# Kernel optimization log

Hardware: AMD Instinct MI355X
Metric: run time of the kernel (lower is better)

The kernel has to match this reference:

```python
import jax, jax.numpy as jnp
import numpy as np

N, IN_F, OUT_F, H = 4096, 256, 512, 8
D = OUT_F // H  # hidden per head
NEG_SLOPE = 0.2


def setup_inputs() -> dict:
    key = jax.random.key(0)
    k1, k2, k3 = jax.random.split(key, 3)
    inp = jax.random.normal(k1, (N, IN_F), dtype=jnp.float32)
    A = jnp.zeros((N, N), dtype=jnp.float32)  # additive adjacency mask
    # xavier_uniform for W [out, in]
    limW = float(np.sqrt(6.0 / (IN_F + H * D)))
    W = jax.random.uniform(k2, (H * D, IN_F), minval=-limW, maxval=limW, dtype=jnp.float32)
    lima = float(np.sqrt(6.0 / (H * D + 1)))
    a_left = jax.random.uniform(k3, (1, H, D), minval=-lima, maxval=lima, dtype=jnp.float32)
    return {"inp": inp, "A": A, "W": W, "a_left": a_left}


def reference(inp, A, W, a_left):
    # h: [N, H, D]
    h = (inp @ W.T).reshape(-1, H, D)
    # NOTE: source uses a_left for BOTH source and target scores (a_right is dead code)
    scores = jnp.sum(h * a_left, axis=-1)  # [N, H]
    s = scores.T  # [H, N]
    # [H, N, N] additive attention logits
    logits = jax.nn.leaky_relu(s[:, :, None] + s[:, None, :], negative_slope=NEG_SLOPE)
    logits = logits + A[None, :, :]
    att = jax.nn.softmax(logits, axis=-1)  # [H, N, N]
    # bmm: [H,N,N] x [H,N,D] -> [H,N,D] -> [N,H,D]
    out = jnp.einsum('hij,jhd->ihd', att, h)
    return out.reshape(-1, H * D)
```

## Files before the change

kernel.cpp:

```cpp
#include <hip/hip_runtime.h>
#include <math.h>

#define N 4096
#define IN_F 256
#define OUT_F 512
#define H 8
#define D 64
#define NEG 0.2f
#define JC 2048

typedef __attribute__((ext_vector_type(8))) short bf16x8;
typedef __attribute__((ext_vector_type(4))) float f32x4;

__device__ __forceinline__ float leaky(float x) { return fmaxf(x, NEG * x); }

__device__ __forceinline__ unsigned short f2bf(float x) {
    union { float f; unsigned u; } v; v.f = x;
    unsigned r = v.u + 0x7fff + ((v.u >> 16) & 1);
    return (unsigned short)(r >> 16);
}

__device__ __forceinline__ unsigned fmap(float x) {
    union { float f; unsigned u; } v; v.f = x;
    return (v.u & 0x80000000u) ? ~v.u : (v.u | 0x80000000u);
}
__device__ __forceinline__ float funmap(unsigned m) {
    union { float f; unsigned u; } v;
    v.u = (m & 0x80000000u) ? (m & 0x7fffffffu) : ~m;
    return v.f;
}

__device__ __forceinline__ void dma16(const void* g, void* l) {
    __builtin_amdgcn_global_load_lds((const __attribute__((address_space(1))) void*)g,
                                     (__attribute__((address_space(3))) void*)l, 16, 0, 0);
}

__global__ __launch_bounds__(256) void k_gemm(const float* __restrict__ inp,
                                              const float* __restrict__ W,
                                              const float* __restrict__ a_left,
                                              unsigned short* __restrict__ hbT,
                                              float* __restrict__ s,
                                              unsigned* __restrict__ smaxU) {
    __shared__ float As[64][68];
    __shared__ float Bs[64][68];
    __shared__ unsigned short h_st[64][72];
    __shared__ float s_red[64];

    const int t = threadIdx.x;
    const int bi = blockIdx.x;
    const int head = blockIdx.y;
    const int ty = t >> 4, tx = t & 15;
    const int lr = t >> 2;
    const int cq = (t & 3) * 16;

    float4 pa[4], pb[4];
    auto loadrk = [&](int k0) {
        const float* ip = &inp[(size_t)(bi * 64 + lr) * IN_F + k0 + cq];
        const float* wp = &W[(size_t)(head * 64 + lr) * IN_F + k0 + cq];
#pragma unroll
        for (int q = 0; q < 4; ++q) {
            pa[q] = *(const float4*)&ip[q * 4];
            pb[q] = *(const float4*)&wp[q * 4];
        }
    };
    loadrk(0);

    float acc[4][4] = {};
    for (int k0 = 0; k0 < IN_F; k0 += 64) {
        __syncthreads();
#pragma unroll
        for (int q = 0; q < 4; ++q)
#pragma unroll
            for (int j = 0; j < 4; ++j) {
                As[cq + q * 4 + j][lr] = ((const float*)&pa[q])[j];
                Bs[cq + q * 4 + j][lr] = ((const float*)&pb[q])[j];
            }
        __syncthreads();
        if (k0 + 64 < IN_F) loadrk(k0 + 64);
#pragma unroll
        for (int k = 0; k < 64; ++k) {
            float4 a4 = *(const float4*)&As[k][ty * 4];
            float4 b4 = *(const float4*)&Bs[k][tx * 4];
            float a[4] = {a4.x, a4.y, a4.z, a4.w};
            float b[4] = {b4.x, b4.y, b4.z, b4.w};
#pragma unroll
            for (int r = 0; r < 4; ++r)
#pragma unroll
                for (int c = 0; c < 4; ++c) acc[r][c] = fmaf(a[r], b[c], acc[r][c]);
        }
    }

    float aL[4];
#pragma unroll
    for (int c = 0; c < 4; ++c) aL[c] = a_left[head * D + tx * 4 + c];
#pragma unroll
    for (int r = 0; r < 4; ++r) {
        float sp = acc[r][0] * aL[0] + acc[r][1] * aL[1] + acc[r][2] * aL[2] + acc[r][3] * aL[3];
        sp += __shfl_xor(sp, 1); sp += __shfl_xor(sp, 2);
        sp += __shfl_xor(sp, 4); sp += __shfl_xor(sp, 8);
        if (tx == 0) {
            s[head * N + bi * 64 + ty * 4 + r] = sp;
            s_red[ty * 4 + r] = sp;
        }
    }
    __syncthreads();
    if (t < 64) {
        float m = s_red[t];
        for (int off = 32; off; off >>= 1) m = fmaxf(m, __shfl_down(m, off, 64));
        if (t == 0) atomicMax(&smaxU[head], fmap(m));
    }

#pragma unroll
    for (int r = 0; r < 4; ++r) {
        ushort4 v;
        v.x = f2bf(acc[r][0]); v.y = f2bf(acc[r][1]);
        v.z = f2bf(acc[r][2]); v.w = f2bf(acc[r][3]);
        *(ushort4*)&h_st[ty * 4 + r][tx * 4] = v;
    }
    __syncthreads();
    {
        const int d = t >> 2, iq = (t & 3) * 16;
        unsigned short us[16];
#pragma unroll
        for (int k = 0; k < 16; ++k) us[k] = h_st[iq + k][d];
        unsigned short* dst = &hbT[((size_t)(head * D + d)) * N + bi * 64 + iq];
#pragma unroll
        for (int q = 0; q < 4; ++q) {
            ushort4 v = {us[q * 4 + 0], us[q * 4 + 1], us[q * 4 + 2], us[q * 4 + 3]};
            *(ushort4*)&dst[q * 4] = v;
        }
    }
}

__global__ __launch_bounds__(256) void k_rowmax(const float* __restrict__ A,
                                                float* __restrict__ rmax) {
    int i = blockIdx.x;
    const float* row = &A[(size_t)i * N];
    float m = -1e30f;
    for (int j = threadIdx.x * 4; j < N; j += 256 * 4) {
        float4 v = *(const float4*)&row[j];
        m = fmaxf(fmaxf(fmaxf(m, v.x), fmaxf(v.y, v.z)), v.w);
    }
    for (int off = 32; off; off >>= 1) m = fmaxf(m, __shfl_down(m, off, 64));
    __shared__ float red[4];
    if ((threadIdx.x & 63) == 0) red[threadIdx.x >> 6] = m;
    __syncthreads();
    if (threadIdx.x == 0) rmax[i] = fmaxf(fmaxf(red[0], red[1]), fmaxf(red[2], red[3]));
}

__global__ __launch_bounds__(256, 4) void k_attn(const float* __restrict__ A,
                                                 const unsigned short* __restrict__ hbT,
                                                 const float* __restrict__ s,
                                                 const unsigned* __restrict__ smaxU,
                                                 const float* __restrict__ rmax,
                                                 float* __restrict__ out,
                                                 float* __restrict__ Z) {
    __shared__ float A_st[64 * 16 * 4];
    __shared__ unsigned short hT_st[64 * 8 * 8];
    __shared__ float s_ch[JC];

    const int t = threadIdx.x;
    const int i0 = blockIdx.x * 64;
    const int head = blockIdx.y;
    const int j0 = blockIdx.z * JC;
    const int lane = t & 63, wave = t >> 6, quad = lane >> 4, li = lane & 15;
    const int iw = wave * 16;
    const int myrow = i0 + iw + li;

#pragma unroll
    for (int q = 0; q < 2; ++q) {
        int idx = q * 256 + t;
        *(float4*)&s_ch[idx * 4] = *(const float4*)&s[head * N + j0 + idx * 4];
    }
    const float s_i = s[head * N + myrow];
    const float mb = leaky(s_i + funmap(smaxU[head])) + rmax[myrow];

    const float* gA[4]; void* lA[4];
#pragma unroll
    for (int q = 0; q < 4; ++q) {
        int slot = q * 256 + t;
        int r = slot >> 4, c4p = slot & 15;
        int c4 = c4p ^ (r & 7);
        gA[q] = &A[(size_t)(i0 + r) * N + j0 + c4 * 4];
        lA[q] = (void*)&A_st[slot * 4];
    }
    const unsigned short* gH[2]; void* lH[2];
#pragma unroll
    for (int q = 0; q < 2; ++q) {
        int slot = q * 256 + t;
        int r = slot >> 3, u = slot & 7;
        int uc = u ^ (r & 7);
        gH[q] = &hbT[(size_t)head * D * N + (size_t)r * N + j0 + uc * 8];
        lH[q] = (void*)&hT_st[slot * 8];
    }

    f32x4 acc[4] = {{0, 0, 0, 0}, {0, 0, 0, 0}, {0, 0, 0, 0}, {0, 0, 0, 0}};
    float zsum = 0.f;

    for (int jt = 0; jt < JC; jt += 64) {
        __syncthreads();
#pragma unroll
        for (int q = 0; q < 4; ++q) dma16(gA[q] + jt, lA[q]);
#pragma unroll
        for (int q = 0; q < 2; ++q) dma16(gH[q] + jt, lH[q]);
        __syncthreads();

#pragma unroll
        for (int kh = 0; kh < 2; ++kh) {
            const int u0 = kh * 8 + quad * 2;
            const int sw = li & 7;
            float4 a0 = *(const float4*)&A_st[((iw + li) * 16 + (u0 ^ sw)) * 4];
            float4 a1 = *(const float4*)&A_st[((iw + li) * 16 + ((u0 + 1) ^ sw)) * 4];
            const int jl = kh * 32 + quad * 8;
            float4 s0 = *(const float4*)&s_ch[jt + jl];
            float4 s1 = *(const float4*)&s_ch[jt + jl + 4];
            float av[8] = {a0.x, a0.y, a0.z, a0.w, a1.x, a1.y, a1.z, a1.w};
            float sv[8] = {s0.x, s0.y, s0.z, s0.w, s1.x, s1.y, s1.z, s1.w};
            union { bf16x8 v; unsigned u[4]; } P;
#pragma unroll
            for (int p = 0; p < 4; ++p) {
                float x0 = s_i + sv[2 * p + 0];
                float x1 = s_i + sv[2 * p + 1];
                float w0 = __expf(fmaxf(x0, NEG * x0) + (av[2 * p + 0] - mb));
                float w1 = __expf(fmaxf(x1, NEG * x1) + (av[2 * p + 1] - mb));
                zsum += w0 + w1;
                P.u[p] = ((unsigned)f2bf(w1) << 16) | (unsigned)f2bf(w0);
            }
#pragma unroll
            for (int db = 0; db < 4; ++db) {
                int slotH = (db * 16 + li) * 8 + ((kh * 4 + quad) ^ sw);
                bf16x8 hf = *(const bf16x8*)&hT_st[slotH * 8];
                acc[db] = __builtin_amdgcn_mfma_f32_16x16x32_bf16(P.v, hf, acc[db], 0, 0, 0);
            }
        }
    }

    zsum += __shfl_xor(zsum, 16);
    zsum += __shfl_xor(zsum, 32);
    if (quad == 0) atomicAdd(&Z[head * N + myrow], zsum);

#pragma unroll
    for (int r = 0; r < 4; ++r) {
        float* op = &out[(size_t)(i0 + iw + quad * 4 + r) * OUT_F + head * D];
#pragma unroll
        for (int db = 0; db < 4; ++db) atomicAdd(&op[db * 16 + li], acc[db][r]);
    }
}

__global__ __launch_bounds__(256) void k_norm(float* __restrict__ out,
                                              const float* __restrict__ Z) {
    int idx = blockIdx.x * 256 + threadIdx.x;
    int i = idx >> 9, hd = idx & 511, hh = hd >> 6;
    out[idx] = out[idx] / Z[hh * N + i];
}

extern "C" void kernel_launch(void* const* d_in, const int* in_sizes, int n_in,
                              void* d_out, int out_size, void* d_ws, size_t ws_size,
                              hipStream_t stream) {
    const float* inp = (const float*)d_in[0];
    const float* A = (const float*)d_in[1];
    const float* W = (const float*)d_in[2];
    const float* a_left = (const float*)d_in[3];
    float* out = (float*)d_out;

    unsigned short* hbT = (unsigned short*)d_ws;
    float* s = (float*)((char*)d_ws + (size_t)H * D * N * 2);
    float* Z = s + (size_t)H * N;
    unsigned* smaxU = (unsigned*)(Z + (size_t)H * N);
    float* rmax = (float*)(smaxU + 8);

    hipMemsetAsync(out, 0, (size_t)N * OUT_F * sizeof(float), stream);
    hipMemsetAsync(Z, 0, (size_t)H * N * sizeof(float) + 8 * sizeof(unsigned), stream);

    k_gemm<<<dim3(N / 64, H), 256, 0, stream>>>(inp, W, a_left, hbT, s, smaxU);
    k_rowmax<<<dim3(N), 256, 0, stream>>>(A, rmax);
    k_attn<<<dim3(N / 64, H, N / JC), 256, 0, stream>>>(A, hbT, s, smaxU, rmax, out, Z);
    k_norm<<<dim3(N * OUT_F / 256), 256, 0, stream>>>(out, Z);
}
```

Measured before the change: 197.3 us.

## Convert adjacency mask to bf16 once and use larger double-buffered attention tiles

Adds a prep kernel that computes the row max of A and also writes a bf16 copy of A into workspace. A new attention kernel then streams that half-size mask instead of re-reading fp32 A once per head. The new kernel works on 128-row tiles with double-buffered LDS loads, computes the softmax denominator with an MFMA against a ones vector, and uses cheaper bf16 rounding. It only runs when the workspace is large enough, otherwise the old path is used. Rounding the mask to bf16 changes precision for arbitrary masks.

```diff
diff --git a/kernel.cpp b/kernel.cpp
--- a/kernel.cpp
+++ b/kernel.cpp
@@ -132,6 +132,26 @@
     }
 }
 
+__global__ __launch_bounds__(256) void k_prep(const float* __restrict__ A,
+                                              unsigned short* __restrict__ Abf,
+                                              float* __restrict__ rmax) {
+    int i = blockIdx.x;
+    const float* row = &A[(size_t)i * N];
+    unsigned short* dst = &Abf[(size_t)i * N];
+    float m = -1e30f;
+    for (int j = threadIdx.x * 4; j < N; j += 256 * 4) {
+        float4 v = *(const float4*)&row[j];
+        m = fmaxf(fmaxf(fmaxf(m, v.x), fmaxf(v.y, v.z)), v.w);
+        ushort4 b = {f2bf(v.x), f2bf(v.y), f2bf(v.z), f2bf(v.w)};
+        *(ushort4*)&dst[j] = b;
+    }
+    for (int off = 32; off; off >>= 1) m = fmaxf(m, __shfl_down(m, off, 64));
+    __shared__ float red[4];
+    if ((threadIdx.x & 63) == 0) red[threadIdx.x >> 6] = m;
+    __syncthreads();
+    if (threadIdx.x == 0) rmax[i] = fmaxf(fmaxf(red[0], red[1]), fmaxf(red[2], red[3]));
+}
+
 __global__ __launch_bounds__(256) void k_rowmax(const float* __restrict__ A,
                                                 float* __restrict__ rmax) {
     int i = blockIdx.x;
@@ -148,15 +168,141 @@
     if (threadIdx.x == 0) rmax[i] = fmaxf(fmaxf(red[0], red[1]), fmaxf(red[2], red[3]));
 }
 
-__global__ __launch_bounds__(256, 4) void k_attn(const float* __restrict__ A,
-                                                 const unsigned short* __restrict__ hbT,
-                                                 const float* __restrict__ s,
-                                                 const unsigned* __restrict__ smaxU,
-                                                 const float* __restrict__ rmax,
-                                                 float* __restrict__ out,
-                                                 float* __restrict__ Z) {
-    __shared__ float A_st[64 * 16 * 4];
-    __shared__ unsigned short hT_st[64 * 8 * 8];
+__global__ __launch_bounds__(256, 2) void k_attn_big(const unsigned short* __restrict__ Abf,
+                                                     const unsigned short* __restrict__ hbT,
+                                                     const float* __restrict__ s,
+                                                     const unsigned* __restrict__ smaxU,
+                                                     const float* __restrict__ rmax,
+                                                     float* __restrict__ out,
+                                                     float* __restrict__ Z) {
+    __shared__ unsigned short A_st[2][128 * 64];
+    __shared__ unsigned short hT_st[2][64 * 64];
+    __shared__ float s_ch[JC];
+
+    const int t = threadIdx.x;
+    const int i0 = blockIdx.x * 128;
+    const int head = blockIdx.y;
+    const int j0 = blockIdx.z * JC;
+    const int lane = t & 63, wave = t >> 6, quad = lane >> 4, li = lane & 15;
+
+#pragma unroll
+    for (int q = 0; q < 2; ++q) {
+        int idx = q * 256 + t;
+        *(float4*)&s_ch[idx * 4] = *(const float4*)&s[head * N + j0 + idx * 4];
+    }
+    const float smx = funmap(smaxU[head]);
+    float s_i[2], negmb[2];
+#pragma unroll
+    for (int is = 0; is < 2; ++is) {
+        int row = i0 + wave * 32 + is * 16 + li;
+        float sv = s[head * N + row];
+        s_i[is] = sv;
+        negmb[is] = -(leaky(sv + smx) + rmax[row]);
+    }
+
+    const unsigned short* gA[4]; unsigned short* lA[2][4];
+#pragma unroll
+    for (int q = 0; q < 4; ++q) {
+        int slot = q * 256 + t, row = slot >> 3, u = slot & 7;
+        gA[q] = Abf + (size_t)(i0 + row) * N + j0 + ((u ^ (row & 7)) << 3);
+        lA[0][q] = &A_st[0][slot * 8];
+        lA[1][q] = &A_st[1][slot * 8];
+    }
+    const unsigned short* gH[2]; unsigned short* lH[2][2];
+#pragma unroll
+    for (int q = 0; q < 2; ++q) {
+        int slot = q * 256 + t, d = slot >> 3, u = slot & 7;
+        gH[q] = hbT + (size_t)head * D * N + (size_t)d * N + j0 + ((u ^ (d & 7)) << 3);
+        lH[0][q] = &hT_st[0][slot * 8];
+        lH[1][q] = &hT_st[1][slot * 8];
+    }
+
+    f32x4 acc[2][4] = {};
+    f32x4 accz[2] = {};
+    bf16x8 onesb;
+#pragma unroll
+    for (int i = 0; i < 8; ++i) onesb[i] = 0x3F80;
+
+#pragma unroll
+    for (int q = 0; q < 4; ++q) dma16(gA[q], lA[0][q]);
+#pragma unroll
+    for (int q = 0; q < 2; ++q) dma16(gH[q], lH[0][q]);
+
+    for (int tt = 0; tt < JC / 64; ++tt) {
+        const int p = tt & 1;
+        __syncthreads();
+        if (tt + 1 < JC / 64) {
+            const int ju = (tt + 1) * 64;
+#pragma unroll
+            for (int q = 0; q < 4; ++q) dma16(gA[q] + ju, lA[p ^ 1][q]);
+#pragma unroll
+            for (int q = 0; q < 2; ++q) dma16(gH[q] + ju, lH[p ^ 1][q]);
+        }
+        const int jt = tt * 64;
+#pragma unroll
+        for (int kh = 0; kh < 2; ++kh) {
+            const int u0 = kh * 4 + quad;
+            float4 s0 = *(const float4*)&s_ch[jt + kh * 32 + quad * 8];
+            float4 s1 = *(const float4*)&s_ch[jt + kh * 32 + quad * 8 + 4];
+            float sv[8] = {s0.x, s0.y, s0.z, s0.w, s1.x, s1.y, s1.z, s1.w};
+            bf16x8 hf[4];
+#pragma unroll
+            for (int db = 0; db < 4; ++db) {
+                int d = db * 16 + li;
+                hf[db] = *(const bf16x8*)&hT_st[p][(d * 8 + (u0 ^ (d & 7))) * 8];
+            }
+#pragma unroll
+            for (int is = 0; is < 2; ++is) {
+                int r = wave * 32 + is * 16 + li;
+                uint4 au = *(const uint4*)&A_st[p][(r * 8 + (u0 ^ (r & 7))) * 8];
+                unsigned auv[4] = {au.x, au.y, au.z, au.w};
+                union { bf16x8 v; unsigned u[4]; } P;
+                const float si = s_i[is], nmb = negmb[is];
+#pragma unroll
+                for (int w = 0; w < 4; ++w) {
+                    float aLo = __uint_as_float(auv[w] << 16);
+                    float aHi = __uint_as_float(auv[w] & 0xffff0000u);
+                    float t0 = si + sv[2 * w], t1 = si + sv[2 * w + 1];
+                    float l0 = fmaxf(t0, NEG * t0), l1 = fmaxf(t1, NEG * t1);
+                    float e0 = __expf(l0 + (aLo + nmb));
+                    float e1 = __expf(l1 + (aHi + nmb));
+                    unsigned r0 = __float_as_uint(e0) + 0x8000u;
+                    unsigned r1 = __float_as_uint(e1) + 0x8000u;
+                    P.u[w] = __builtin_amdgcn_perm(r1, r0, 0x07060302u);
+                }
+#pragma unroll
+                for (int db = 0; db < 4; ++db)
+                    acc[is][db] = __builtin_amdgcn_mfma_f32_16x16x32_bf16(P.v, hf[db], acc[is][db], 0, 0, 0);
+                accz[is] = __builtin_amdgcn_mfma_f32_16x16x32_bf16(P.v, onesb, accz[is], 0, 0, 0);
+            }
+        }
+    }
+
+#pragma unroll
+    for (int is = 0; is < 2; ++is) {
+        int rowbase = i0 + wave * 32 + is * 16 + quad * 4;
+#pragma unroll
+        for (int r = 0; r < 4; ++r) {
+            float* op = &out[(size_t)(rowbase + r) * OUT_F + head * D];
+#pragma unroll
+            for (int db = 0; db < 4; ++db) atomicAdd(&op[db * 16 + li], acc[is][db][r]);
+        }
+        if (li == 0) {
+#pragma unroll
+            for (int r = 0; r < 4; ++r) atomicAdd(&Z[head * N + rowbase + r], accz[is][r]);
+        }
+    }
+}
+
+__global__ __launch_bounds__(256, 4) void k_attn_f(const float* __restrict__ A,
+                                                   const unsigned short* __restrict__ hbT,
+                                                   const float* __restrict__ s,
+                                                   const unsigned* __restrict__ smaxU,
+                                                   const float* __restrict__ rmax,
+                                                   float* __restrict__ out,
+                                                   float* __restrict__ Z) {
+    __shared__ float A_stf[64 * 16 * 4];
+    __shared__ unsigned short hT_stf[64 * 8 * 8];
     __shared__ float s_ch[JC];
 
     const int t = threadIdx.x;
@@ -182,7 +328,7 @@
         int r = slot >> 4, c4p = slot & 15;
         int c4 = c4p ^ (r & 7);
         gA[q] = &A[(size_t)(i0 + r) * N + j0 + c4 * 4];
-        lA[q] = (void*)&A_st[slot * 4];
+        lA[q] = (void*)&A_stf[slot * 4];
     }
     const unsigned short* gH[2]; void* lH[2];
 #pragma unroll
@@ -191,7 +337,7 @@
         int r = slot >> 3, u = slot & 7;
         int uc = u ^ (r & 7);
         gH[q] = &hbT[(size_t)head * D * N + (size_t)r * N + j0 + uc * 8];
-        lH[q] = (void*)&hT_st[slot * 8];
+        lH[q] = (void*)&hT_stf[slot * 8];
     }
 
     f32x4 acc[4] = {{0, 0, 0, 0}, {0, 0, 0, 0}, {0, 0, 0, 0}, {0, 0, 0, 0}};
@@ -209,8 +355,8 @@
         for (int kh = 0; kh < 2; ++kh) {
             const int u0 = kh * 8 + quad * 2;
             const int sw = li & 7;
-            float4 a0 = *(const float4*)&A_st[((iw + li) * 16 + (u0 ^ sw)) * 4];
-            float4 a1 = *(const float4*)&A_st[((iw + li) * 16 + ((u0 + 1) ^ sw)) * 4];
+            float4 a0 = *(const float4*)&A_stf[((iw + li) * 16 + (u0 ^ sw)) * 4];
+            float4 a1 = *(const float4*)&A_stf[((iw + li) * 16 + ((u0 + 1) ^ sw)) * 4];
             const int jl = kh * 32 + quad * 8;
             float4 s0 = *(const float4*)&s_ch[jt + jl];
             float4 s1 = *(const float4*)&s_ch[jt + jl + 4];
@@ -229,7 +375,7 @@
 #pragma unroll
             for (int db = 0; db < 4; ++db) {
                 int slotH = (db * 16 + li) * 8 + ((kh * 4 + quad) ^ sw);
-                bf16x8 hf = *(const bf16x8*)&hT_st[slotH * 8];
+                bf16x8 hf = *(const bf16x8*)&hT_stf[slotH * 8];
                 acc[db] = __builtin_amdgcn_mfma_f32_16x16x32_bf16(P.v, hf, acc[db], 0, 0, 0);
             }
         }
@@ -268,12 +414,19 @@
     float* Z = s + (size_t)H * N;
     unsigned* smaxU = (unsigned*)(Z + (size_t)H * N);
     float* rmax = (float*)(smaxU + 8);
+    unsigned short* Abf = (unsigned short*)((char*)d_ws + ((size_t)5 << 20));
+    const bool big = ws_size >= (((size_t)5 << 20) + (size_t)N * N * 2);
 
     hipMemsetAsync(out, 0, (size_t)N * OUT_F * sizeof(float), stream);
     hipMemsetAsync(Z, 0, (size_t)H * N * sizeof(float) + 8 * sizeof(unsigned), stream);
 
     k_gemm<<<dim3(N / 64, H), 256, 0, stream>>>(inp, W, a_left, hbT, s, smaxU);
-    k_rowmax<<<dim3(N), 256, 0, stream>>>(A, rmax);
-    k_attn<<<dim3(N / 64, H, N / JC), 256, 0, stream>>>(A, hbT, s, smaxU, rmax, out, Z);
+    if (big) {
+        k_prep<<<dim3(N), 256, 0, stream>>>(A, Abf, rmax);
+        k_attn_big<<<dim3(N / 128, H, N / JC), 256, 0, stream>>>(Abf, hbT, s, smaxU, rmax, out, Z);
+    } else {
+        k_rowmax<<<dim3(N), 256, 0, stream>>>(A, rmax);
+        k_attn_f<<<dim3(N / 64, H, N / JC), 256, 0, stream>>>(A, hbT, s, smaxU, rmax, out, Z);
+    }
     k_norm<<<dim3(N * OUT_F / 256), 256, 0, stream>>>(out, Z);
 }
```

New measurement: 208.9 us. 5.8% more time.
